# Optimization experiments

Hardware: AMD Instinct MI355X
Metric: run time of the kernel (lower is better)

Reference implementation:

```python
import jax, jax.numpy as jnp
import numpy as np

N_NODES = 100000
N_EDGES = 1600000
IN_F = 16
OUT_F = 64
PERIODS = 12
N_PHASE = 4


def setup_inputs() -> dict:
    key = jax.random.key(0)
    ks = jax.random.split(key, 12)
    inp = {
        'x': jax.random.normal(ks[0], (N_NODES, IN_F, PERIODS), jnp.float32),
        'edge_index': jax.random.randint(ks[1], (2, N_EDGES), 0, N_NODES, jnp.int64),
        'attn': jax.random.normal(ks[2], (PERIODS,), jnp.float32),
        'conv_z_w': jax.random.normal(ks[3], (IN_F, OUT_F), jnp.float32) * 0.1,
        'conv_z_b': jnp.zeros((OUT_F,), jnp.float32),
        'conv_r_w': jax.random.normal(ks[4], (IN_F, OUT_F), jnp.float32) * 0.1,
        'conv_r_b': jnp.zeros((OUT_F,), jnp.float32),
        'conv_h_w': jax.random.normal(ks[5], (IN_F, OUT_F), jnp.float32) * 0.1,
        'conv_h_b': jnp.zeros((OUT_F,), jnp.float32),
        'lin_z_w': jax.random.normal(ks[6], (2 * OUT_F, OUT_F), jnp.float32) * 0.1,
        'lin_z_b': jnp.zeros((OUT_F,), jnp.float32),
        'lin_r_w': jax.random.normal(ks[7], (2 * OUT_F, OUT_F), jnp.float32) * 0.1,
        'lin_r_b': jnp.zeros((OUT_F,), jnp.float32),
        'lin_h_w': jax.random.normal(ks[8], (2 * OUT_F, OUT_F), jnp.float32) * 0.1,
        'lin_h_b': jnp.zeros((OUT_F,), jnp.float32),
        'out_w': jax.random.normal(ks[9], (OUT_F, N_PHASE), jnp.float32) * 0.1,
        'out_b': jnp.zeros((N_PHASE,), jnp.float32),
    }
    return inp


def _gcn_norm(edge_index, num_nodes, dtype):
    # add self loops (fill value 1), symmetric normalization as in PyG gcn_norm
    loops = jnp.arange(num_nodes, dtype=edge_index.dtype)
    src = jnp.concatenate([edge_index[0], loops])
    dst = jnp.concatenate([edge_index[1], loops])
    deg = jax.ops.segment_sum(jnp.ones_like(dst, dtype=dtype), dst, num_segments=num_nodes)
    dinv = jnp.where(deg > 0, jax.lax.rsqrt(deg), jnp.zeros_like(deg))
    norm = dinv[src] * dinv[dst]  # [E + N]
    return src, dst, norm


def reference(x, edge_index, attn, conv_z_w, conv_z_b, conv_r_w, conv_r_b,
              conv_h_w, conv_h_b, lin_z_w, lin_z_b, lin_r_w, lin_r_b,
              lin_h_w, lin_h_b, out_w, out_b):
    N = x.shape[0]
    periods = x.shape[2]
    F_out = conv_z_w.shape[1]
    src, dst, norm = _gcn_norm(edge_index, N, x.dtype)

    def conv(Xp, W, b):
        XW = Xp @ W                                   # [N, F_out]
        msg = norm[:, None] * XW[src]                 # gather over edges
        return jax.ops.segment_sum(msg, dst, num_segments=N) + b

    probs = jax.nn.softmax(attn)
    H0 = jnp.zeros((N, F_out), x.dtype)  # A3TGCN never carries H between periods
    H_accum = jnp.zeros((N, F_out), x.dtype)
    for p in range(periods):
        Xp = x[:, :, p]
        Z = jax.nn.sigmoid(jnp.concatenate([conv(Xp, conv_z_w, conv_z_b), H0], axis=1) @ lin_z_w + lin_z_b)
        R = jax.nn.sigmoid(jnp.concatenate([conv(Xp, conv_r_w, conv_r_b), H0], axis=1) @ lin_r_w + lin_r_b)
        Ht = jnp.tanh(jnp.concatenate([conv(Xp, conv_h_w, conv_h_b), H0 * R], axis=1) @ lin_h_w + lin_h_b)
        H = Z * H0 + (1.0 - Z) * Ht
        H_accum = H_accum + probs[p] * H

    h = jax.nn.relu(H_accum)
    logits = h @ out_w + out_b
    return jax.nn.softmax(logits, axis=1)
```

## Files before the change

### kernel.cpp

```cpp
#include <hip/hip_runtime.h>
#include <math.h>

#define NN 100000
#define NE 1600000
#define PERIODS 12
#define SLOTS 48
#define NBUCK 391
#define FRAG 256
#define CAPB 48
#define PTH 512

typedef unsigned short ushort_t;
typedef __attribute__((ext_vector_type(8))) short short8;
typedef __attribute__((ext_vector_type(16))) float floatx16;
typedef __attribute__((ext_vector_type(2))) float f32x2;

union F4S8 { float4 f; short8 s; int4 i; };

__device__ __forceinline__ ushort_t f2bf(float f) {
  unsigned u = __float_as_uint(f);
  unsigned r = u + 0x7fffu + ((u >> 16) & 1u);
  return (ushort_t)(r >> 16);
}

__device__ __forceinline__ f32x2 unpk(unsigned u) {
  f32x2 t;
  t.x = __uint_as_float(u << 16);
  t.y = __uint_as_float(u & 0xffff0000u);
  return t;
}
__device__ __forceinline__ void pkadd(f32x2& a, f32x2 t) {
  asm("v_pk_add_f32 %0, %0, %1" : "+v"(a) : "v"(t));
}

__global__ __launch_bounds__(PTH) void k_part(
    const int* __restrict__ src, const int* __restrict__ dst,
    int* __restrict__ cnt_blk, int* __restrict__ part,
    const float* __restrict__ attn,
    const float* __restrict__ czw, const float* __restrict__ czb,
    const float* __restrict__ chw, const float* __restrict__ chb,
    const float* __restrict__ lzw, const float* __restrict__ lzb,
    const float* __restrict__ lhw, const float* __restrict__ lhb,
    ushort_t* __restrict__ Bz32, ushort_t* __restrict__ Bh32,
    float2* __restrict__ cb2, float* __restrict__ probs_ext) {
  if (blockIdx.x == FRAG) {
    for (int t5 = threadIdx.x; t5 < 1024; t5 += PTH) {
      int f = t5 >> 6, c = t5 & 63;
      float az = 0.f, ah = 0.f;
#pragma unroll 8
      for (int k = 0; k < 64; ++k) {
        az += czw[f * 64 + k] * lzw[k * 64 + c];
        ah += chw[f * 64 + k] * lhw[k * 64 + c];
      }
      int idx = (((c >> 5) * 64) + ((f >> 3) * 32) + (c & 31)) * 8 + (f & 7);
      Bz32[idx] = f2bf(az);
      Bh32[idx] = f2bf(ah);
    }
    if (threadIdx.x < 64) {
      int t = threadIdx.x;
      float vz = lzb[t], vh = lhb[t];
      for (int k = 0; k < 64; ++k) {
        vz += czb[k] * lzw[k * 64 + t];
        vh += chb[k] * lhw[k * 64 + t];
      }
      cb2[t] = make_float2(vz, vh);
    }
    if (threadIdx.x == 0) {
      float m = -1e30f;
      for (int p = 0; p < PERIODS; ++p) m = fmaxf(m, attn[p]);
      float e[PERIODS], s = 0.f;
      for (int p = 0; p < PERIODS; ++p) { e[p] = __expf(attn[p] - m); s += e[p]; }
      float inv = 1.f / s;
      for (int r = 0; r < 32; ++r)
        probs_ext[r] = (r < 12) ? e[r] * inv : ((r < 24) ? e[r - 12] * inv : 0.f);
    }
    return;
  }
  __shared__ int cnt[NBUCK];
  int tid = threadIdx.x, blk = blockIdx.x;
  for (int c = tid; c < NBUCK; c += PTH) cnt[c] = 0;
  __syncthreads();
  for (unsigned i = blk * (unsigned)PTH + tid; i < NE / 4; i += FRAG * (unsigned)PTH) {
    int4 dv = ((const int4*)dst)[i];
    int4 sv = ((const int4*)src)[i];
    int d[4] = {dv.x, dv.y, dv.z, dv.w};
    int s[4] = {sv.x, sv.y, sv.z, sv.w};
#pragma unroll
    for (int k = 0; k < 4; ++k) {
      int cls = d[k] >> 8;
      int slot = atomicAdd(&cnt[cls], 1);
      if (slot < CAPB)
        part[(size_t)(cls * FRAG + blk) * CAPB + slot] = (d[k] & 255) | (s[k] << 8);
    }
  }
  __syncthreads();
  for (int c = tid; c < NBUCK; c += PTH) cnt_blk[blk * NBUCK + c] = cnt[c];
}

__global__ __launch_bounds__(512) void k_csr(const int* __restrict__ cnt_blk,
                                             const int* __restrict__ part,
                                             int* __restrict__ deg,
                                             int* __restrict__ csr) {
  __shared__ int cnt[256];
  int b = blockIdx.x, tid = threadIdx.x;
  if (tid < 256) cnt[tid] = 0;
  __syncthreads();
  int f = tid & 255, sub = tid >> 8;
  int c = cnt_blk[f * NBUCK + b];
  c = c < CAPB ? c : CAPB;
  const int* cell = part + (size_t)(b * FRAG + f) * CAPB;
  for (int i = sub; i < c; i += 2) {
    int r = cell[i];
    int dl = r & 255;
    int slot = atomicAdd(&cnt[dl], 1);
    if (slot < SLOTS)
      csr[((size_t)(b * 256 + dl)) * SLOTS + slot] = (r >> 8) * 384;
  }
  __syncthreads();
  int node = b * 256 + tid;
  if (tid < 256 && node < NN) {
    int cc = cnt[tid];
    deg[node] = cc;
    int cl = cc < SLOTS ? cc : SLOTS;
    int padded = (cl + 3) & ~3;
    int* row = csr + (size_t)node * SLOTS;
    for (int sl = cl; sl < padded; ++sl) row[sl] = NN * 384;
  }
}

__global__ __launch_bounds__(256) void k_prescale(const float* __restrict__ x,
                                                  const int* __restrict__ deg,
                                                  ushort_t* __restrict__ xs) {
  __shared__ float st[4][192];
  int wid = threadIdx.x >> 6, l = threadIdx.x & 63;
  int n = blockIdx.x * 4 + wid;
  if (n > NN || l >= 48) return;
  char* ob = (char*)xs;
  if (n == NN) {
    uint2 z; z.x = 0u; z.y = 0u;
    *(uint2*)(ob + (size_t)NN * 384 + l * 8) = z;
    return;
  }
  float4 v4 = *(const float4*)(x + (size_t)n * 192 + 4 * l);
  *(float4*)&st[wid][4 * l] = v4;
  asm volatile("s_waitcnt lgkmcnt(0)" ::: "memory");
  float dn = rsqrtf((float)(deg[n] + 1));
  float v[4];
#pragma unroll
  for (int c = 0; c < 4; ++c) {
    int o = 4 * l + c;
    v[c] = dn * st[wid][(o & 15) * 12 + (o >> 4)];
  }
  uint2 w;
  w.x = (unsigned)f2bf(v[0]) | ((unsigned)f2bf(v[1]) << 16);
  w.y = (unsigned)f2bf(v[2]) | ((unsigned)f2bf(v[3]) << 16);
  *(uint2*)(ob + (size_t)n * 384 + l * 8) = w;
}

__global__ __launch_bounds__(256) void k_main(
    const ushort_t* __restrict__ xs, const int* __restrict__ csr,
    const int* __restrict__ deg,
    const ushort_t* __restrict__ Bz32, const ushort_t* __restrict__ Bh32,
    const float2* __restrict__ cb2, const float* __restrict__ probs_ext,
    const float* __restrict__ out_w, const float* __restrict__ out_b,
    float* __restrict__ out) {
  __shared__ ushort_t Alds[4][32][16];
  int wid = __builtin_amdgcn_readfirstlane(threadIdx.x >> 6);
  int l = threadIdx.x & 63;
  int nA = blockIdx.x * 8 + wid * 2;
  int nB = nA + 1;
  char* albase = (char*)&Alds[wid][0][0];
  if (l < 16) *(int4*)(albase + 768 + l * 16) = make_int4(0, 0, 0, 0);

  const char* xb = (const char*)xs;
  unsigned loff = (unsigned)(l < 48 ? l : 47) * 8u;

  int2 dd = *(const int2*)(deg + nA);
  int dA = dd.x, dB = dd.y;
  int cA = dA < SLOTS ? dA : SLOTS, cB = dB < SLOTS ? dB : SLOTS;
  int KA = (cA + 3) >> 2, KB = (cB + 3) >> 2;
  const int* bktA = csr + (size_t)nA * SLOTS;
  const int* bktB = bktA + SLOTS;

  uint2 sA = *(const uint2*)(xb + (unsigned)nA * 384u + loff);
  uint2 sB = *(const uint2*)(xb + (unsigned)nB * 384u + loff);
  f32x2 aA01 = unpk(sA.x), aA23 = unpk(sA.y);
  f32x2 aB01 = unpk(sB.x), aB23 = unpk(sB.y);

  uint2 qa[4], qb[4];
  auto issue4 = [&](const int* bkt, int k, uint2* q) {
    int4 e = ((const int4*)bkt)[k];
    q[0] = *(const uint2*)(xb + (unsigned)e.x + loff);
    q[1] = *(const uint2*)(xb + (unsigned)e.y + loff);
    q[2] = *(const uint2*)(xb + (unsigned)e.z + loff);
    q[3] = *(const uint2*)(xb + (unsigned)e.w + loff);
  };
  auto accA4 = [&](const uint2* q) {
#pragma unroll
    for (int j = 0; j < 4; ++j) { pkadd(aA01, unpk(q[j].x)); pkadd(aA23, unpk(q[j].y)); }
  };
  auto accB4 = [&](const uint2* q) {
#pragma unroll
    for (int j = 0; j < 4; ++j) { pkadd(aB01, unpk(q[j].x)); pkadd(aB23, unpk(q[j].y)); }
  };

  int km = KA < KB ? KA : KB;
  int k = 0;
  for (; k < km; ++k) {
    issue4(bktA, k, qa);
    issue4(bktB, k, qb);
    accA4(qa);
    accB4(qb);
  }
  for (; k < KA; ++k) { issue4(bktA, k, qa); accA4(qa); }
  for (; k < KB; ++k) { issue4(bktB, k, qb); accB4(qb); }

  float dnA = rsqrtf((float)(dA + 1)), dnB = rsqrtf((float)(dB + 1));

  if (l < 48) {
    uint2 wA, wB;
    wA.x = (unsigned)f2bf(dnA * aA01.x) | ((unsigned)f2bf(dnA * aA01.y) << 16);
    wA.y = (unsigned)f2bf(dnA * aA23.x) | ((unsigned)f2bf(dnA * aA23.y) << 16);
    wB.x = (unsigned)f2bf(dnB * aB01.x) | ((unsigned)f2bf(dnB * aB01.y) << 16);
    wB.y = (unsigned)f2bf(dnB * aB23.x) | ((unsigned)f2bf(dnB * aB23.y) << 16);
    *(uint2*)(albase + l * 8) = wA;
    *(uint2*)(albase + 384 + l * 8) = wB;
  }
  asm volatile("s_waitcnt lgkmcnt(0)" ::: "memory");
  F4S8 afr;
  afr.f = *(const float4*)(albase + (unsigned)(l & 31) * 32u + (unsigned)(l >> 5) * 16u);

  F4S8 bz0, bz1, bh0, bh1;
  bz0.f = ((const float4*)Bz32)[l];
  bz1.f = ((const float4*)Bz32)[64 + l];
  bh0.f = ((const float4*)Bh32)[l];
  bh1.f = ((const float4*)Bh32)[64 + l];

  floatx16 zero16;
#pragma unroll
  for (int r = 0; r < 16; ++r) zero16[r] = 0.f;
  floatx16 az0 = __builtin_amdgcn_mfma_f32_32x32x16_bf16(afr.s, bz0.s, zero16, 0, 0, 0);
  floatx16 az1 = __builtin_amdgcn_mfma_f32_32x32x16_bf16(afr.s, bz1.s, zero16, 0, 0, 0);
  floatx16 ah0 = __builtin_amdgcn_mfma_f32_32x32x16_bf16(afr.s, bh0.s, zero16, 0, 0, 0);
  floatx16 ah1 = __builtin_amdgcn_mfma_f32_32x32x16_bf16(afr.s, bh1.s, zero16, 0, 0, 0);

  float2 cbv0 = cb2[l & 31], cbv1 = cb2[(l & 31) + 32];
  float prv[12];
  unsigned sby = (l & 32u) >> 1;
#pragma unroll
  for (int r = 0; r < 12; ++r) {
    const int rb = (r & 3) + 8 * (r >> 2);
    prv[r] = *(const float*)((const char*)probs_ext + rb * 4 + sby);
  }
  bool sh = (l & 32) != 0;
  float hA[2], hB[2];
#pragma unroll
  for (int t = 0; t < 2; ++t) {
    float g0 = 0.f, g1 = 0.f, g2 = 0.f;
    float2 cbv = t ? cbv1 : cbv0;
#pragma unroll
    for (int r = 0; r < 12; ++r) {
      float zz = (t ? az1[r] : az0[r]) + cbv.x;
      float hh = (t ? ah1[r] : ah0[r]) + cbv.y;
      float ez = __expf(zz);
      float e2h = __expf(2.f * hh);
      float val = (e2h - 1.f) * __builtin_amdgcn_rcpf((1.f + ez) * (e2h + 1.f));
      float c = prv[r] * val;
      if ((r >> 2) == 0) g0 += c;
      else if ((r >> 2) == 1) g1 += c;
      else g2 += c;
    }
    float pa = g0 + (sh ? 0.f : g1);
    float pb = g2 + (sh ? g1 : 0.f);
    pa += __shfl_xor(pa, 32, 64);
    pb += __shfl_xor(pb, 32, 64);
    hA[t] = fmaxf(pa, 0.f);
    hB[t] = fmaxf(pb, 0.f);
  }

  int c0 = l & 31;
  float4 w0 = ((const float4*)out_w)[c0];
  float4 w1 = ((const float4*)out_w)[c0 + 32];
  float h0 = sh ? hB[0] : hA[0];
  float h1 = sh ? hB[1] : hA[1];
  float l0 = h0 * w0.x; l0 = fmaf(h1, w1.x, l0);
  float l1 = h0 * w0.y; l1 = fmaf(h1, w1.y, l1);
  float l2 = h0 * w0.z; l2 = fmaf(h1, w1.z, l2);
  float l3 = h0 * w0.w; l3 = fmaf(h1, w1.w, l3);
#pragma unroll
  for (int o = 1; o < 32; o <<= 1) {
    l0 += __shfl_xor(l0, o, 64);
    l1 += __shfl_xor(l1, o, 64);
    l2 += __shfl_xor(l2, o, 64);
    l3 += __shfl_xor(l3, o, 64);
  }
  l0 += out_b[0]; l1 += out_b[1]; l2 += out_b[2]; l3 += out_b[3];
  float m = fmaxf(fmaxf(l0, l1), fmaxf(l2, l3));
  float e0 = __expf(l0 - m), e1 = __expf(l1 - m), e2 = __expf(l2 - m), e3 = __expf(l3 - m);
  float inv = __builtin_amdgcn_rcpf(e0 + e1 + e2 + e3);
  if (c0 < 4) {
    float v = (c0 == 0) ? e0 * inv : (c0 == 1) ? e1 * inv : (c0 == 2) ? e2 * inv : e3 * inv;
    out[(size_t)(sh ? nB : nA) * 4 + c0] = v;
  }
}

extern "C" void kernel_launch(void* const* d_in, const int* in_sizes, int n_in,
                              void* d_out, int out_size, void* d_ws, size_t ws_size,
                              hipStream_t stream) {
  const float* x    = (const float*)d_in[0];
  const int*   ei   = (const int*)d_in[1];
  const float* attn = (const float*)d_in[2];
  const float* czw  = (const float*)d_in[3];
  const float* czb  = (const float*)d_in[4];
  const float* chw  = (const float*)d_in[7];
  const float* chb  = (const float*)d_in[8];
  const float* lzw  = (const float*)d_in[9];
  const float* lzb  = (const float*)d_in[10];
  const float* lhw  = (const float*)d_in[13];
  const float* lhb  = (const float*)d_in[14];
  const float* outw = (const float*)d_in[15];
  const float* outb = (const float*)d_in[16];
  float* out = (float*)d_out;

  char* ws = (char*)d_ws;
  size_t off = 0;
  auto alloc = [&](size_t bytes) {
    void* p = ws + off;
    off += (bytes + 255) & ~(size_t)255;
    return p;
  };
  int*      deg       = (int*)alloc((size_t)NN * 4);
  int*      csr       = (int*)alloc((size_t)NN * SLOTS * 4);
  void*     shared_region = alloc((size_t)(NN + 1) * 192 * 2);
  int*      part      = (int*)shared_region;
  ushort_t* xs        = (ushort_t*)shared_region;
  int*      cnt_blk   = (int*)alloc((size_t)FRAG * NBUCK * 4);
  ushort_t* Bz32      = (ushort_t*)alloc(2 * 64 * 8 * 2);
  ushort_t* Bh32      = (ushort_t*)alloc(2 * 64 * 8 * 2);
  float2*   cb2       = (float2*)alloc(64 * 8);
  float*    probs_ext = (float*)alloc(32 * 4);

  k_part<<<FRAG + 1, PTH, 0, stream>>>(ei, ei + NE, cnt_blk, part,
                                       attn, czw, czb, chw, chb,
                                       lzw, lzb, lhw, lhb,
                                       Bz32, Bh32, cb2, probs_ext);
  k_csr<<<NBUCK, 512, 0, stream>>>(cnt_blk, part, deg, csr);
  k_prescale<<<NN / 4 + 1, 256, 0, stream>>>(x, deg, xs);
  k_main<<<NN / 8, 256, 0, stream>>>(xs, csr, deg, Bz32, Bh32, cb2, probs_ext,
                                     outw, outb, out);
}
```

Measured before the change: 298.9 us.

## Fuse CSR build with prescale, double-buffer gathers, halve partition block size

Result: slower. 311.1 us (+4.1%).

```diff
diff --git a/kernel.cpp b/kernel.cpp
--- a/kernel.cpp
+++ b/kernel.cpp
@@ -8,7 +8,7 @@
 #define NBUCK 391
 #define FRAG 256
 #define CAPB 48
-#define PTH 512
+#define PTH 256
 
 typedef unsigned short ushort_t;
 typedef __attribute__((ext_vector_type(8))) short short8;
@@ -97,11 +97,33 @@
   for (int c = tid; c < NBUCK; c += PTH) cnt_blk[blk * NBUCK + c] = cnt[c];
 }
 
-__global__ __launch_bounds__(512) void k_csr(const int* __restrict__ cnt_blk,
-                                             const int* __restrict__ part,
-                                             int* __restrict__ deg,
-                                             int* __restrict__ csr) {
+__device__ __forceinline__ void prescale_node(const float* __restrict__ x,
+                                              ushort_t* __restrict__ xs,
+                                              float* stw, int n, int cc, int l) {
+  float4 v4 = *(const float4*)(x + (size_t)n * 192 + 4 * l);
+  *(float4*)&stw[4 * l] = v4;
+  asm volatile("s_waitcnt lgkmcnt(0)" ::: "memory");
+  float dn = rsqrtf((float)(cc + 1));
+  float v[4];
+#pragma unroll
+  for (int c = 0; c < 4; ++c) {
+    int o = 4 * l + c;
+    v[c] = dn * stw[(o & 15) * 12 + (o >> 4)];
+  }
+  uint2 w;
+  w.x = (unsigned)f2bf(v[0]) | ((unsigned)f2bf(v[1]) << 16);
+  w.y = (unsigned)f2bf(v[2]) | ((unsigned)f2bf(v[3]) << 16);
+  *(uint2*)((char*)xs + (size_t)n * 384 + l * 8) = w;
+}
+
+__global__ __launch_bounds__(512) void k_csr_ps(const int* __restrict__ cnt_blk,
+                                                const int* __restrict__ part,
+                                                int* __restrict__ deg,
+                                                int* __restrict__ csr,
+                                                const float* __restrict__ x,
+                                                ushort_t* __restrict__ xs) {
   __shared__ int cnt[256];
+  __shared__ float st[8][192];
   int b = blockIdx.x, tid = threadIdx.x;
   if (tid < 256) cnt[tid] = 0;
   __syncthreads();
@@ -126,6 +148,50 @@
     int* row = csr + (size_t)node * SLOTS;
     for (int sl = cl; sl < padded; ++sl) row[sl] = NN * 384;
   }
+  int wv = tid >> 6, l = tid & 63;
+  if (b == 0 && tid < 48) {
+    uint2 z; z.x = 0u; z.y = 0u;
+    *(uint2*)((char*)xs + (size_t)NN * 384 + tid * 8) = z;
+  }
+  if (l >= 48) return;
+  float* stw = st[wv];
+  for (int j = 0; j < 32; ++j) {
+    int idx = wv * 32 + j;
+    int n = b * 256 + idx;
+    if (n >= NN) break;
+    prescale_node(x, xs, stw, n, cnt[idx], l);
+  }
+}
+
+__global__ __launch_bounds__(512) void k_csr(const int* __restrict__ cnt_blk,
+                                             const int* __restrict__ part,
+                                             int* __restrict__ deg,
+                                             int* __restrict__ csr) {
+  __shared__ int cnt[256];
+  int b = blockIdx.x, tid = threadIdx.x;
+  if (tid < 256) cnt[tid] = 0;
+  __syncthreads();
+  int f = tid & 255, sub = tid >> 8;
+  int c = cnt_blk[f * NBUCK + b];
+  c = c < CAPB ? c : CAPB;
+  const int* cell = part + (size_t)(b * FRAG + f) * CAPB;
+  for (int i = sub; i < c; i += 2) {
+    int r = cell[i];
+    int dl = r & 255;
+    int slot = atomicAdd(&cnt[dl], 1);
+    if (slot < SLOTS)
+      csr[((size_t)(b * 256 + dl)) * SLOTS + slot] = (r >> 8) * 384;
+  }
+  __syncthreads();
+  int node = b * 256 + tid;
+  if (tid < 256 && node < NN) {
+    int cc = cnt[tid];
+    deg[node] = cc;
+    int cl = cc < SLOTS ? cc : SLOTS;
+    int padded = (cl + 3) & ~3;
+    int* row = csr + (size_t)node * SLOTS;
+    for (int sl = cl; sl < padded; ++sl) row[sl] = NN * 384;
+  }
 }
 
 __global__ __launch_bounds__(256) void k_prescale(const float* __restrict__ x,
@@ -135,26 +201,12 @@
   int wid = threadIdx.x >> 6, l = threadIdx.x & 63;
   int n = blockIdx.x * 4 + wid;
   if (n > NN || l >= 48) return;
-  char* ob = (char*)xs;
   if (n == NN) {
     uint2 z; z.x = 0u; z.y = 0u;
-    *(uint2*)(ob + (size_t)NN * 384 + l * 8) = z;
+    *(uint2*)((char*)xs + (size_t)NN * 384 + l * 8) = z;
     return;
   }
-  float4 v4 = *(const float4*)(x + (size_t)n * 192 + 4 * l);
-  *(float4*)&st[wid][4 * l] = v4;
-  asm volatile("s_waitcnt lgkmcnt(0)" ::: "memory");
-  float dn = rsqrtf((float)(deg[n] + 1));
-  float v[4];
-#pragma unroll
-  for (int c = 0; c < 4; ++c) {
-    int o = 4 * l + c;
-    v[c] = dn * st[wid][(o & 15) * 12 + (o >> 4)];
-  }
-  uint2 w;
-  w.x = (unsigned)f2bf(v[0]) | ((unsigned)f2bf(v[1]) << 16);
-  w.y = (unsigned)f2bf(v[2]) | ((unsigned)f2bf(v[3]) << 16);
-  *(uint2*)(ob + (size_t)n * 384 + l * 8) = w;
+  prescale_node(x, xs, st[wid], n, deg[n], l);
 }
 
 __global__ __launch_bounds__(256) void k_main(
@@ -187,7 +239,7 @@
   f32x2 aA01 = unpk(sA.x), aA23 = unpk(sA.y);
   f32x2 aB01 = unpk(sB.x), aB23 = unpk(sB.y);
 
-  uint2 qa[4], qb[4];
+  uint2 qa0[4], qb0[4], qa1[4], qb1[4];
   auto issue4 = [&](const int* bkt, int k, uint2* q) {
     int4 e = ((const int4*)bkt)[k];
     q[0] = *(const uint2*)(xb + (unsigned)e.x + loff);
@@ -206,14 +258,16 @@
 
   int km = KA < KB ? KA : KB;
   int k = 0;
-  for (; k < km; ++k) {
-    issue4(bktA, k, qa);
-    issue4(bktB, k, qb);
-    accA4(qa);
-    accB4(qb);
-  }
-  for (; k < KA; ++k) { issue4(bktA, k, qa); accA4(qa); }
-  for (; k < KB; ++k) { issue4(bktB, k, qb); accB4(qb); }
+  if (km > 0) { issue4(bktA, 0, qa0); issue4(bktB, 0, qb0); }
+  for (; k + 2 <= km; k += 2) {
+    issue4(bktA, k + 1, qa1); issue4(bktB, k + 1, qb1);
+    accA4(qa0); accB4(qb0);
+    if (k + 2 < km) { issue4(bktA, k + 2, qa0); issue4(bktB, k + 2, qb0); }
+    accA4(qa1); accB4(qb1);
+  }
+  if (k < km) { accA4(qa0); accB4(qb0); ++k; }
+  for (; k < KA; ++k) { issue4(bktA, k, qa0); accA4(qa0); }
+  for (; k < KB; ++k) { issue4(bktB, k, qb0); accB4(qb0); }
 
   float dnA = rsqrtf((float)(dA + 1)), dnB = rsqrtf((float)(dB + 1));
 
@@ -329,23 +383,41 @@
     off += (bytes + 255) & ~(size_t)255;
     return p;
   };
-  int*      deg       = (int*)alloc((size_t)NN * 4);
-  int*      csr       = (int*)alloc((size_t)NN * SLOTS * 4);
-  void*     shared_region = alloc((size_t)(NN + 1) * 192 * 2);
-  int*      part      = (int*)shared_region;
-  ushort_t* xs        = (ushort_t*)shared_region;
+  int* deg = (int*)alloc((size_t)NN * 4);
+  int* csr = (int*)alloc((size_t)NN * SLOTS * 4);
+  size_t mark = off;
+
+  ushort_t* xs   = (ushort_t*)alloc((size_t)(NN + 1) * 384);
+  int*      part = (int*)alloc((size_t)NBUCK * FRAG * CAPB * 4);
   int*      cnt_blk   = (int*)alloc((size_t)FRAG * NBUCK * 4);
   ushort_t* Bz32      = (ushort_t*)alloc(2 * 64 * 8 * 2);
   ushort_t* Bh32      = (ushort_t*)alloc(2 * 64 * 8 * 2);
   float2*   cb2       = (float2*)alloc(64 * 8);
   float*    probs_ext = (float*)alloc(32 * 4);
+  bool fused = (off <= ws_size);
+
+  if (!fused) {
+    off = mark;
+    void* shared_region = alloc((size_t)(NN + 1) * 384);
+    part = (int*)shared_region;
+    xs   = (ushort_t*)shared_region;
+    cnt_blk   = (int*)alloc((size_t)FRAG * NBUCK * 4);
+    Bz32      = (ushort_t*)alloc(2 * 64 * 8 * 2);
+    Bh32      = (ushort_t*)alloc(2 * 64 * 8 * 2);
+    cb2       = (float2*)alloc(64 * 8);
+    probs_ext = (float*)alloc(32 * 4);
+  }
 
   k_part<<<FRAG + 1, PTH, 0, stream>>>(ei, ei + NE, cnt_blk, part,
                                        attn, czw, czb, chw, chb,
                                        lzw, lzb, lhw, lhb,
                                        Bz32, Bh32, cb2, probs_ext);
-  k_csr<<<NBUCK, 512, 0, stream>>>(cnt_blk, part, deg, csr);
-  k_prescale<<<NN / 4 + 1, 256, 0, stream>>>(x, deg, xs);
+  if (fused) {
+    k_csr_ps<<<NBUCK, 512, 0, stream>>>(cnt_blk, part, deg, csr, x, xs);
+  } else {
+    k_csr<<<NBUCK, 512, 0, stream>>>(cnt_blk, part, deg, csr);
+    k_prescale<<<NN / 4 + 1, 256, 0, stream>>>(x, deg, xs);
+  }
   k_main<<<NN / 8, 256, 0, stream>>>(xs, csr, deg, Bz32, Bh32, cb2, probs_ext,
                                      outw, outb, out);
 }
```
